# Kernel optimization log

Measured on AMD Instinct MI355X. Metric: run time of the kernel, lower is better.

The kernel has to match this reference:

```python
import jax, jax.numpy as jnp
import numpy as np

B, S, HID = 1, 4096, 2048
NH, NKV, D = 16, 4, 128           # num_heads, num_kv_heads, head_dim
QPG = NH // NKV                   # q heads per kv group
GROUP = (QPG + 2) * D             # fused per-group width: Q..Q K V
TOTAL = NKV * GROUP


def setup_inputs() -> dict:
    key = jax.random.key(0)
    k0, k1, k2 = jax.random.split(key, 3)
    x = jax.random.normal(k0, (B, S, HID), dtype=jnp.float32)
    weight_qkv = jax.random.normal(k1, (TOTAL, HID), dtype=jnp.float32) * 0.02
    weight_proj = jax.random.normal(k2, (HID, NH * D), dtype=jnp.float32) * 0.02
    return {"x": x, "weight_qkv": weight_qkv, "weight_proj": weight_proj}


def reference(x, weight_qkv, weight_proj):
    b, s, _ = x.shape
    # fused QKV projection, grouped layout: [b, s, NKV, (QPG+2)*D]
    qkv = jnp.einsum('bsh,ph->bsp', x, weight_qkv).reshape(b, s, NKV, GROUP)
    q = qkv[..., : QPG * D].reshape(b, s, NKV, QPG, D)      # [b,s,g,q,d]
    k = qkv[..., QPG * D:(QPG + 1) * D]                      # [b,s,g,d]
    v = qkv[..., (QPG + 1) * D:]                             # [b,s,g,d]

    scale = 1.0 / jnp.sqrt(jnp.float32(D))
    # GQA causal attention (ring attention at cp_size=1 == full causal attn)
    scores = jnp.einsum('bsgqd,btgd->bgqst', q, k) * scale   # [b,g,q,s,s]
    causal = jnp.tril(jnp.ones((s, s), dtype=bool))
    scores = jnp.where(causal, scores, jnp.finfo(scores.dtype).min)
    attn = jax.nn.softmax(scores, axis=-1)
    out = jnp.einsum('bgqst,btgd->bsgqd', attn, v)           # [b,s,g,q,d]
    out = out.reshape(b, s, NH * D)
    return jnp.einsum('bse,he->bsh', out, weight_proj)       # [b,s,HID]
```

## Files before the change

kernel.cpp:

```cpp
#include <hip/hip_runtime.h>
#include <hip/hip_bf16.h>
#include <stdint.h>

typedef __attribute__((ext_vector_type(8))) short short8;
typedef __attribute__((ext_vector_type(4))) float f32x4;

#define S_LEN   4096
#define HID_DIM 2048
#define NHEAD   16
#define NKV     4
#define DHEAD   128
#define QPG     4
#define GROUP   768
#define TOTAL   3072

#define NSLOT   256

__device__ __forceinline__ ushort f2bf(float f) {
    union { float f; uint32_t u; } c; c.f = f;
    uint32_t u = c.u;
    u += 0x7fff + ((u >> 16) & 1);
    return (ushort)(u >> 16);
}

__device__ __forceinline__ void gld_lds16(const void* g, void* l) {
    __builtin_amdgcn_global_load_lds(
        (const __attribute__((address_space(1))) void*)g,
        (__attribute__((address_space(3))) void*)l, 16, 0, 0);
}

__global__ __launch_bounds__(256)
void cvt_f32_bf16(const float* __restrict__ src, ushort* __restrict__ dst,
                  int n4, int mode)
{
    int i = blockIdx.x * blockDim.x + threadIdx.x;
    int stride = gridDim.x * blockDim.x;
    for (; i < n4; i += stride) {
        float sc = 1.0f;
        if (mode == 1) {
            int row = i >> 9;
            sc = ((row % GROUP) < QPG * DHEAD) ? 0.088388347648318447f : 1.0f;
        }
        float4 v = ((const float4*)src)[i];
        ushort4 o;
        o.x = f2bf(v.x * sc); o.y = f2bf(v.y * sc);
        o.z = f2bf(v.z * sc); o.w = f2bf(v.w * sc);
        ((ushort4*)dst)[i] = o;
    }
}

__global__ __launch_bounds__(256)
void zero_f4(float4* __restrict__ p, int n4)
{
    int i = blockIdx.x * blockDim.x + threadIdx.x;
    int stride = gridDim.x * blockDim.x;
    float4 z = {0.f, 0.f, 0.f, 0.f};
    for (; i < n4; i += stride) p[i] = z;
}

__device__ __forceinline__ void store_c(ushort* C, size_t idx, float v) { C[idx] = f2bf(v); }
__device__ __forceinline__ void store_c(float*  C, size_t idx, float v) { C[idx] = v; }

template <typename OutT, bool WRITE_VT>
__global__ __launch_bounds__(256, 2)
void gemm_bt(const ushort* __restrict__ A, const ushort* __restrict__ B,
             OutT* __restrict__ C, ushort* __restrict__ VT,
             int M, int N, int K)
{
    __shared__ alignas(16) ushort Asl[128 * 32];
    __shared__ alignas(16) ushort Bsl[128 * 32];

    const int tid  = threadIdx.x;
    const int wave = tid >> 6;
    const int lane = tid & 63;
    const int quad = lane >> 4;
    const int l15  = lane & 15;
    const int wr   = wave >> 1;
    const int wc   = wave & 1;
    const int m0   = blockIdx.y * 128;
    const int n0   = blockIdx.x * 128;

    f32x4 acc[4][4];
#pragma unroll
    for (int i = 0; i < 4; i++)
#pragma unroll
        for (int j = 0; j < 4; j++) acc[i][j] = (f32x4)0.0f;

    for (int kb = 0; kb < K; kb += 32) {
        __syncthreads();
#pragma unroll
        for (int r = 0; r < 2; r++) {
            int idx = tid + r * 256;
            int row = idx >> 2, c8 = idx & 3;
            char* la = (char*)Asl + (size_t)(wave * 64 + r * 256) * 16;
            char* lb = (char*)Bsl + (size_t)(wave * 64 + r * 256) * 16;
            gld_lds16(A + (size_t)(m0 + row) * K + kb + c8 * 8, la);
            gld_lds16(B + (size_t)(n0 + row) * K + kb + c8 * 8, lb);
        }
        __syncthreads();

        short8 af[4], bf[4];
#pragma unroll
        for (int i = 0; i < 4; i++)
            af[i] = *(const short8*)(&Asl[(wr * 64 + i * 16 + l15) * 32 + quad * 8]);
#pragma unroll
        for (int j = 0; j < 4; j++)
            bf[j] = *(const short8*)(&Bsl[(wc * 64 + j * 16 + l15) * 32 + quad * 8]);
#pragma unroll
        for (int i = 0; i < 4; i++)
#pragma unroll
            for (int j = 0; j < 4; j++)
                acc[i][j] = __builtin_amdgcn_mfma_f32_16x16x32_bf16(
                    af[i], bf[j], acc[i][j], 0, 0, 0);
    }

#pragma unroll
    for (int i = 0; i < 4; i++)
#pragma unroll
        for (int j = 0; j < 4; j++)
#pragma unroll
            for (int r = 0; r < 4; r++) {
                int row = m0 + wr * 64 + i * 16 + quad * 4 + r;
                int col = n0 + wc * 64 + j * 16 + l15;
                store_c(C, (size_t)row * N + col, acc[i][j][r]);
            }

    if (WRITE_VT) {
        int cb = n0 >> 7;
        if (cb % 6 == 5) {
            int g = cb / 6;
#pragma unroll
            for (int i = 0; i < 4; i++)
#pragma unroll
                for (int j = 0; j < 4; j++) {
                    int d    = wc * 64 + j * 16 + l15;
                    int row0 = m0 + wr * 64 + i * 16 + quad * 4;
                    ushort4 pk;
                    pk.x = f2bf(acc[i][j][0]); pk.y = f2bf(acc[i][j][1]);
                    pk.z = f2bf(acc[i][j][2]); pk.w = f2bf(acc[i][j][3]);
                    *(ushort4*)(VT + (size_t)(g * 128 + d) * S_LEN + row0) = pk;
                }
        }
    }
}

__global__ __launch_bounds__(256, 2)
void flash_attn(const ushort* __restrict__ qkv, const ushort* __restrict__ VT,
                ushort* __restrict__ out, float* __restrict__ o_slot,
                float* __restrict__ l_slot)
{
    const int b    = blockIdx.x;
    const int head = b >> 5;
    const int pair = (b >> 1) & 15;
    const int half = b & 1;
    const int g    = head >> 2;
    const int qh   = head & 3;
    const int H    = 128 - 4 * pair;
    const int L    = 4 * pair + 4;
    const int slot = head * 16 + pair;

    const int tid  = threadIdx.x;
    const int wave = tid >> 6;
    const int lane = tid & 63;
    const int quad = lane >> 4;
    const int l15  = lane & 15;

    __shared__ alignas(16) ushort Kl[2][32][136];
    __shared__ alignas(16) ushort Vt[2][128][40];
    __shared__ alignas(16) ushort Pl[4][32][36];

    int seg_p[2], seg_t0[2], seg_t1[2], seg_part[2];
    int nseg;
    if (half == 0) {
        nseg = 1;
        seg_p[0] = 31 - pair; seg_t0[0] = 0;  seg_t1[0] = 66; seg_part[0] = 1;
    } else {
        nseg = 2;
        seg_p[0] = 31 - pair; seg_t0[0] = 66; seg_t1[0] = H;  seg_part[0] = 1;
        seg_p[1] = pair;      seg_t0[1] = 0;  seg_t1[1] = L;  seg_part[1] = 0;
    }

    const int koff = g * GROUP + QPG * DHEAD;

    for (int s = 0; s < nseg; s++) {
        const int t0 = seg_t0[s];
        const int t1 = seg_t1[s];
        const int q0 = seg_p[s] * 128;

        short8 qf[2][4];
#pragma unroll
        for (int mi = 0; mi < 2; mi++) {
            int row = q0 + wave * 32 + mi * 16 + l15;
            const ushort* qp = qkv + (size_t)row * TOTAL + g * GROUP + qh * DHEAD + quad * 8;
#pragma unroll
            for (int ks = 0; ks < 4; ks++)
                qf[mi][ks] = *(const short8*)(qp + ks * 32);
        }

        f32x4 o[2][8];
#pragma unroll
        for (int mi = 0; mi < 2; mi++)
#pragma unroll
            for (int df = 0; df < 8; df++) o[mi][df] = (f32x4)0.0f;
        float l_vec[2][4];
#pragma unroll
        for (int mi = 0; mi < 2; mi++)
#pragma unroll
            for (int r = 0; r < 4; r++) l_vec[mi][r] = 0.0f;

        const int kr = tid >> 4, kc = tid & 15;
        const int vd = tid >> 2, vc = tid & 3;

        float4 kpre[2], vpre[2];
#pragma unroll
        for (int r = 0; r < 2; r++) {
            kpre[r] = *(const float4*)(qkv + (size_t)(t0 * 32 + kr + r * 16) * TOTAL + koff + kc * 8);
            vpre[r] = *(const float4*)(VT + (size_t)(g * 128 + vd + r * 64) * S_LEN + t0 * 32 + vc * 8);
        }
#pragma unroll
        for (int r = 0; r < 2; r++) {
            *(float4*)(&Kl[0][kr + r * 16][kc * 8]) = kpre[r];
            *(float4*)(&Vt[0][vd + r * 64][vc * 8]) = vpre[r];
        }
        if (t0 + 1 < t1) {
            const int j1 = (t0 + 1) * 32;
#pragma unroll
            for (int r = 0; r < 2; r++) {
                kpre[r] = *(const float4*)(qkv + (size_t)(j1 + kr + r * 16) * TOTAL + koff + kc * 8);
                vpre[r] = *(const float4*)(VT + (size_t)(g * 128 + vd + r * 64) * S_LEN + j1 + vc * 8);
            }
        }
        __syncthreads();

        for (int t = t0; t < t1; t++) {
            const int cur = (t - t0) & 1;

            if (t + 1 < t1) {
#pragma unroll
                for (int r = 0; r < 2; r++) {
                    *(float4*)(&Kl[cur ^ 1][kr + r * 16][kc * 8]) = kpre[r];
                    *(float4*)(&Vt[cur ^ 1][vd + r * 64][vc * 8]) = vpre[r];
                }
                if (t + 2 < t1) {
                    const int j2 = (t + 2) * 32;
#pragma unroll
                    for (int r = 0; r < 2; r++) {
                        kpre[r] = *(const float4*)(qkv + (size_t)(j2 + kr + r * 16) * TOTAL + koff + kc * 8);
                        vpre[r] = *(const float4*)(VT + (size_t)(g * 128 + vd + r * 64) * S_LEN + j2 + vc * 8);
                    }
                }
            }

            const int j0 = t * 32;
            f32x4 sacc[2][2];
#pragma unroll
            for (int mi = 0; mi < 2; mi++)
#pragma unroll
                for (int ni = 0; ni < 2; ni++) sacc[mi][ni] = (f32x4)0.0f;
            __builtin_amdgcn_s_setprio(1);
#pragma unroll
            for (int ni = 0; ni < 2; ni++)
#pragma unroll
                for (int ks = 0; ks < 4; ks++) {
                    short8 kf = *(const short8*)(&Kl[cur][ni * 16 + l15][ks * 32 + quad * 8]);
#pragma unroll
                    for (int mi = 0; mi < 2; mi++)
                        sacc[mi][ni] = __builtin_amdgcn_mfma_f32_16x16x32_bf16(
                            qf[mi][ks], kf, sacc[mi][ni], 0, 0, 0);
                }
            __builtin_amdgcn_s_setprio(0);

#pragma unroll
            for (int mi = 0; mi < 2; mi++) {
                const int base = q0 + wave * 32 + mi * 16;
                if (j0 + 31 > base) {
#pragma unroll
                    for (int r = 0; r < 4; r++) {
                        int row_g = base + quad * 4 + r;
                        float rs = 0.0f;
#pragma unroll
                        for (int ni = 0; ni < 2; ni++) {
                            float e = __expf(sacc[mi][ni][r]);
                            int col_g = j0 + ni * 16 + l15;
                            e = (col_g > row_g) ? 0.0f : e;
                            sacc[mi][ni][r] = e;
                            rs += e;
                        }
                        l_vec[mi][r] += rs;
                    }
                } else {
#pragma unroll
                    for (int r = 0; r < 4; r++) {
                        float rs = 0.0f;
#pragma unroll
                        for (int ni = 0; ni < 2; ni++) {
                            float e = __expf(sacc[mi][ni][r]);
                            sacc[mi][ni][r] = e;
                            rs += e;
                        }
                        l_vec[mi][r] += rs;
                    }
                }
#pragma unroll
                for (int ni = 0; ni < 2; ni++)
#pragma unroll
                    for (int r = 0; r < 4; r++)
                        Pl[wave][mi * 16 + quad * 4 + r][ni * 16 + l15] =
                            f2bf(sacc[mi][ni][r]);
            }

            short8 pf[2];
#pragma unroll
            for (int mi = 0; mi < 2; mi++)
                pf[mi] = *(const short8*)(&Pl[wave][mi * 16 + l15][quad * 8]);
            __builtin_amdgcn_s_setprio(1);
#pragma unroll
            for (int df = 0; df < 8; df++) {
                short8 vf = *(const short8*)(&Vt[cur][df * 16 + l15][quad * 8]);
#pragma unroll
                for (int mi = 0; mi < 2; mi++)
                    o[mi][df] = __builtin_amdgcn_mfma_f32_16x16x32_bf16(
                        pf[mi], vf, o[mi][df], 0, 0, 0);
            }
            __builtin_amdgcn_s_setprio(0);

            __syncthreads();
        }

        if (seg_part[s]) {
#pragma unroll
            for (int mi = 0; mi < 2; mi++)
#pragma unroll
                for (int r = 0; r < 4; r++) {
                    int row_l = wave * 32 + mi * 16 + quad * 4 + r;
                    float l = l_vec[mi][r];
                    l += __shfl_xor(l, 1);
                    l += __shfl_xor(l, 2);
                    l += __shfl_xor(l, 4);
                    l += __shfl_xor(l, 8);
                    if (l15 == 0)
                        atomicAdd(&l_slot[slot * 128 + row_l], l);
#pragma unroll
                    for (int df = 0; df < 8; df++)
                        atomicAdd(&o_slot[((size_t)slot * 128 + row_l) * 128
                                          + df * 16 + l15], o[mi][df][r]);
                }
        } else {
#pragma unroll
            for (int mi = 0; mi < 2; mi++)
#pragma unroll
                for (int r = 0; r < 4; r++) {
                    float l = l_vec[mi][r];
                    l += __shfl_xor(l, 1);
                    l += __shfl_xor(l, 2);
                    l += __shfl_xor(l, 4);
                    l += __shfl_xor(l, 8);
                    float inv = 1.0f / l;
                    int row = q0 + wave * 32 + mi * 16 + quad * 4 + r;
#pragma unroll
                    for (int df = 0; df < 8; df++) {
                        float v = o[mi][df][r] * inv;
                        out[(size_t)row * (NHEAD * DHEAD) + head * DHEAD
                            + df * 16 + l15] = f2bf(v);
                    }
                }
        }
    }
}

__global__ __launch_bounds__(256)
void fixup_norm(const float* __restrict__ o_slot, const float* __restrict__ l_slot,
                ushort* __restrict__ attn)
{
    const int slot = blockIdx.x;
    const int head = slot >> 4;
    const int q0   = (31 - (slot & 15)) * 128;
    const int t    = threadIdx.x;
#pragma unroll 4
    for (int i = 0; i < 64; i++) {
        int idx = i * 256 + t;
        int row = idx >> 7, d = idx & 127;
        float l = l_slot[slot * 128 + row];
        float v = o_slot[(size_t)slot * 16384 + idx] / l;
        attn[(size_t)(q0 + row) * HID_DIM + head * DHEAD + d] = f2bf(v);
    }
}

extern "C" void kernel_launch(void* const* d_in, const int* in_sizes, int n_in,
                              void* d_out, int out_size, void* d_ws, size_t ws_size,
                              hipStream_t stream)
{
    const float* x     = (const float*)d_in[0];
    const float* wqkv  = (const float*)d_in[1];
    const float* wproj = (const float*)d_in[2];
    float* outp = (float*)d_out;

    const size_t n_x     = (size_t)S_LEN * HID_DIM;
    const size_t n_wqkv  = (size_t)TOTAL * HID_DIM;
    const size_t n_wproj = (size_t)HID_DIM * HID_DIM;
    const size_t n_qkv   = (size_t)S_LEN * TOTAL;
    const size_t n_attn  = (size_t)S_LEN * HID_DIM;

    ushort* xb     = (ushort*)d_ws;
    ushort* wqkvb  = xb + n_x;
    ushort* qkv    = wqkvb + n_wqkv;
    ushort* attn   = qkv + n_qkv;
    ushort* vt     = attn + n_attn;
    float* o_slot  = (float*)xb;
    float* l_slot  = (float*)wqkvb;
    ushort* wprojb = wqkvb;

    cvt_f32_bf16<<<2048, 256, 0, stream>>>(x, xb, (int)(n_x / 4), 0);
    cvt_f32_bf16<<<2048, 256, 0, stream>>>(wqkv, wqkvb, (int)(n_wqkv / 4), 1);

    gemm_bt<ushort, true><<<dim3(TOTAL / 128, S_LEN / 128), 256, 0, stream>>>(
        xb, wqkvb, qkv, vt, S_LEN, TOTAL, HID_DIM);

    zero_f4<<<1024, 256, 0, stream>>>((float4*)o_slot, 256 * 16384 / 4);
    zero_f4<<<64, 256, 0, stream>>>((float4*)l_slot, 256 * 128 / 4);

    flash_attn<<<512, 256, 0, stream>>>(qkv, vt, attn, o_slot, l_slot);
    fixup_norm<<<NSLOT, 256, 0, stream>>>(o_slot, l_slot, attn);

    cvt_f32_bf16<<<2048, 256, 0, stream>>>(wproj, wprojb, (int)(n_wproj / 4), 0);
    gemm_bt<float, false><<<dim3(HID_DIM / 128, S_LEN / 128), 256, 0, stream>>>(
        attn, wprojb, outp, nullptr, S_LEN, HID_DIM, HID_DIM);
}
```

Measured before the change: 409.7 us.

## Split causal attention work into three equal chunks per pair and swizzle LDS tiles

Each head's paired query tiles (long and short causal rows, 132 key tiles total) are now split across three blocks of 44 key tiles each instead of two uneven halves, giving 768 blocks with more balanced work. Additional partial slots are added for short tiles that get split, with fixup handling both slot ranges. Separately, K and V shared-memory tiles drop their padding and use XOR swizzling to avoid bank conflicts while saving LDS. The change adds more atomic accumulation traffic and a larger zeroed scratch buffer.

```diff
diff --git a/kernel.cpp b/kernel.cpp
--- a/kernel.cpp
+++ b/kernel.cpp
@@ -14,7 +14,7 @@
 #define GROUP   768
 #define TOTAL   3072
 
-#define NSLOT   256
+#define NSLOT   336
 
 __device__ __forceinline__ ushort f2bf(float f) {
     union { float f; uint32_t u; } c; c.f = f;
@@ -149,15 +149,18 @@
                 ushort* __restrict__ out, float* __restrict__ o_slot,
                 float* __restrict__ l_slot)
 {
-    const int b    = blockIdx.x;
-    const int head = b >> 5;
-    const int pair = (b >> 1) & 15;
-    const int half = b & 1;
+    const int b     = blockIdx.x;
+    const int head  = b / 48;
+    const int r48   = b - head * 48;
+    const int pair  = r48 / 3;
+    const int third = r48 - pair * 3;
+
     const int g    = head >> 2;
     const int qh   = head & 3;
     const int H    = 128 - 4 * pair;
     const int L    = 4 * pair + 4;
-    const int slot = head * 16 + pair;
+    const int c0   = third * 44;
+    const int c1   = c0 + 44;
 
     const int tid  = threadIdx.x;
     const int wave = tid >> 6;
@@ -165,19 +168,27 @@
     const int quad = lane >> 4;
     const int l15  = lane & 15;
 
-    __shared__ alignas(16) ushort Kl[2][32][136];
-    __shared__ alignas(16) ushort Vt[2][128][40];
+    __shared__ alignas(16) ushort Kl[2][32][128];
+    __shared__ alignas(16) ushort Vt[2][128][32];
     __shared__ alignas(16) ushort Pl[4][32][36];
 
-    int seg_p[2], seg_t0[2], seg_t1[2], seg_part[2];
-    int nseg;
-    if (half == 0) {
-        nseg = 1;
-        seg_p[0] = 31 - pair; seg_t0[0] = 0;  seg_t1[0] = 66; seg_part[0] = 1;
-    } else {
-        nseg = 2;
-        seg_p[0] = 31 - pair; seg_t0[0] = 66; seg_t1[0] = H;  seg_part[0] = 1;
-        seg_p[1] = pair;      seg_t0[1] = 0;  seg_t1[1] = L;  seg_part[1] = 0;
+    int seg_p[2], seg_t0[2], seg_t1[2], seg_slot[2];
+    int nseg = 0;
+    {
+        int h1 = (c1 < H) ? c1 : H;
+        if (c0 < h1) {
+            seg_p[nseg] = 31 - pair; seg_t0[nseg] = c0; seg_t1[nseg] = h1;
+            seg_slot[nseg] = head * 16 + pair;
+            nseg++;
+        }
+        int l0 = (c0 > H) ? c0 : H;
+        if (l0 < c1) {
+            int lt0 = l0 - H, lt1 = c1 - H;
+            int whole = (lt0 == 0) & (lt1 == L);
+            seg_p[nseg] = pair; seg_t0[nseg] = lt0; seg_t1[nseg] = lt1;
+            seg_slot[nseg] = whole ? -1 : (256 + head * 5 + (pair - 11));
+            nseg++;
+        }
     }
 
     const int koff = g * GROUP + QPG * DHEAD;
@@ -219,8 +230,9 @@
         }
 #pragma unroll
         for (int r = 0; r < 2; r++) {
-            *(float4*)(&Kl[0][kr + r * 16][kc * 8]) = kpre[r];
-            *(float4*)(&Vt[0][vd + r * 64][vc * 8]) = vpre[r];
+            int krow = kr + r * 16, vrow = vd + r * 64;
+            *(float4*)(&Kl[0][krow][(kc ^ (krow & 7)) * 8]) = kpre[r];
+            *(float4*)(&Vt[0][vrow][(vc ^ (vrow & 3)) * 8]) = vpre[r];
         }
         if (t0 + 1 < t1) {
             const int j1 = (t0 + 1) * 32;
@@ -238,8 +250,9 @@
             if (t + 1 < t1) {
 #pragma unroll
                 for (int r = 0; r < 2; r++) {
-                    *(float4*)(&Kl[cur ^ 1][kr + r * 16][kc * 8]) = kpre[r];
-                    *(float4*)(&Vt[cur ^ 1][vd + r * 64][vc * 8]) = vpre[r];
+                    int krow = kr + r * 16, vrow = vd + r * 64;
+                    *(float4*)(&Kl[cur ^ 1][krow][(kc ^ (krow & 7)) * 8]) = kpre[r];
+                    *(float4*)(&Vt[cur ^ 1][vrow][(vc ^ (vrow & 3)) * 8]) = vpre[r];
                 }
                 if (t + 2 < t1) {
                     const int j2 = (t + 2) * 32;
@@ -262,7 +275,8 @@
             for (int ni = 0; ni < 2; ni++)
 #pragma unroll
                 for (int ks = 0; ks < 4; ks++) {
-                    short8 kf = *(const short8*)(&Kl[cur][ni * 16 + l15][ks * 32 + quad * 8]);
+                    int krow = ni * 16 + l15;
+                    short8 kf = *(const short8*)(&Kl[cur][krow][((ks * 4 + quad) ^ (krow & 7)) * 8]);
 #pragma unroll
                     for (int mi = 0; mi < 2; mi++)
                         sacc[mi][ni] = __builtin_amdgcn_mfma_f32_16x16x32_bf16(
@@ -316,7 +330,8 @@
             __builtin_amdgcn_s_setprio(1);
 #pragma unroll
             for (int df = 0; df < 8; df++) {
-                short8 vf = *(const short8*)(&Vt[cur][df * 16 + l15][quad * 8]);
+                int vrow = df * 16 + l15;
+                short8 vf = *(const short8*)(&Vt[cur][vrow][(quad ^ (vrow & 3)) * 8]);
 #pragma unroll
                 for (int mi = 0; mi < 2; mi++)
                     o[mi][df] = __builtin_amdgcn_mfma_f32_16x16x32_bf16(
@@ -327,7 +342,8 @@
             __syncthreads();
         }
 
-        if (seg_part[s]) {
+        if (seg_slot[s] >= 0) {
+            const int sslot = seg_slot[s];
 #pragma unroll
             for (int mi = 0; mi < 2; mi++)
 #pragma unroll
@@ -339,10 +355,10 @@
                     l += __shfl_xor(l, 4);
                     l += __shfl_xor(l, 8);
                     if (l15 == 0)
-                        atomicAdd(&l_slot[slot * 128 + row_l], l);
+                        atomicAdd(&l_slot[sslot * 128 + row_l], l);
 #pragma unroll
                     for (int df = 0; df < 8; df++)
-                        atomicAdd(&o_slot[((size_t)slot * 128 + row_l) * 128
+                        atomicAdd(&o_slot[((size_t)sslot * 128 + row_l) * 128
                                           + df * 16 + l15], o[mi][df][r]);
                 }
         } else {
@@ -373,9 +389,16 @@
                 ushort* __restrict__ attn)
 {
     const int slot = blockIdx.x;
-    const int head = slot >> 4;
-    const int q0   = (31 - (slot & 15)) * 128;
-    const int t    = threadIdx.x;
+    int head, q0;
+    if (slot < 256) {
+        head = slot >> 4;
+        q0   = (31 - (slot & 15)) * 128;
+    } else {
+        int s = slot - 256;
+        head = s / 5;
+        q0   = (11 + (s - head * 5)) * 128;
+    }
+    const int t = threadIdx.x;
 #pragma unroll 4
     for (int i = 0; i < 64; i++) {
         int idx = i * 256 + t;
@@ -406,8 +429,8 @@
     ushort* qkv    = wqkvb + n_wqkv;
     ushort* attn   = qkv + n_qkv;
     ushort* vt     = attn + n_attn;
-    float* o_slot  = (float*)xb;
-    float* l_slot  = (float*)wqkvb;
+    float* o_slot  = (float*)d_ws;
+    float* l_slot  = o_slot + (size_t)NSLOT * 16384;
     ushort* wprojb = wqkvb;
 
     cvt_f32_bf16<<<2048, 256, 0, stream>>>(x, xb, (int)(n_x / 4), 0);
@@ -416,10 +439,10 @@
     gemm_bt<ushort, true><<<dim3(TOTAL / 128, S_LEN / 128), 256, 0, stream>>>(
         xb, wqkvb, qkv, vt, S_LEN, TOTAL, HID_DIM);
 
-    zero_f4<<<1024, 256, 0, stream>>>((float4*)o_slot, 256 * 16384 / 4);
-    zero_f4<<<64, 256, 0, stream>>>((float4*)l_slot, 256 * 128 / 4);
-
-    flash_attn<<<512, 256, 0, stream>>>(qkv, vt, attn, o_slot, l_slot);
+    zero_f4<<<2048, 256, 0, stream>>>((float4*)o_slot,
+                                      (int)(((size_t)NSLOT * 16384 + NSLOT * 128) / 4));
+
+    flash_attn<<<768, 256, 0, stream>>>(qkv, vt, attn, o_slot, l_slot);
     fixup_norm<<<NSLOT, 256, 0, stream>>>(o_slot, l_slot, attn);
 
     cvt_f32_bf16<<<2048, 256, 0, stream>>>(wproj, wprojb, (int)(n_wproj / 4), 0);
```

Result: slower. 456.6 us (+11.5%).
